# Performance work log

Measured on AMD Instinct MI355X. Metric: run time of the kernel, lower is better.

The kernel has to match this reference:

```python
import jax, jax.numpy as jnp
import numpy as np

B, S, D = 4, 16, 512          # batch, seq, attention_dim
V, T = 32000, 18              # vocab_size, tree_depth
INNER = V - 1                 # internal nodes of Huffman tree


def setup_inputs() -> dict:
    key = jax.random.key(0)
    k_att, k_w, k_idx, k_bit = jax.random.split(key, 4)
    att = jax.random.normal(k_att, (B, S, D), dtype=jnp.float32)
    weight = jax.random.normal(k_w, (INNER, D), dtype=jnp.float32) * 0.02
    path_index = jax.random.randint(k_idx, (V * T,), 0, INNER, dtype=jnp.int64)
    # left/right branch bits: sign=+1,bias=0 -> p ; sign=-1,bias=1 -> 1-p
    bits = jax.random.randint(k_bit, (V * T,), 0, 2).astype(jnp.float32)
    path_sign = 1.0 - 2.0 * bits
    path_bias = bits
    return {
        "att": att,
        "weight": weight,
        "path_index": path_index,
        "path_sign": path_sign,
        "path_bias": path_bias,
        "vocab_size": V,
        "tree_depth": T,
    }


def reference(att, weight, path_index, path_sign, path_bias, vocab_size, tree_depth):
    # h: sigmoid of linear projection onto internal-node vectors  [B,S,INNER]
    h = jax.nn.sigmoid(jnp.einsum("bsd,nd->bsn", att, weight))
    # gather per-(token,depth) internal-node probs, flip via sign/bias
    g = jnp.take(h, path_index, axis=-1) * path_sign + path_bias  # [B,S,V*T]
    Hm = g.reshape(att.shape[0], -1, vocab_size, tree_depth)      # [B,S,V,T]
    return jnp.sum(jnp.log(Hm), axis=-1)                          # [B,S,V]
```

## Files before the change

kernel.cpp:

```cpp
#include <hip/hip_runtime.h>

#define BS    64
#define DDIM  512
#define NV    32000
#define TD    18
#define INNER 31999

typedef __attribute__((ext_vector_type(8))) short short8;
typedef __attribute__((ext_vector_type(4))) float floatx4;

__device__ __forceinline__ float bf16_to_f32(unsigned short u) {
    union { unsigned int i; float f; } v; v.i = ((unsigned int)u) << 16; return v.f;
}
__device__ __forceinline__ unsigned short f32_to_bf16(float f) {
    union { float f; unsigned int i; } v; v.f = f;
    unsigned int r = v.i + 0x7FFFu + ((v.i >> 16) & 1u);
    return (unsigned short)(r >> 16);
}
__device__ __forceinline__ short8 cvt8(float4 a, float4 b) {
    short8 s;
    s[0] = (short)f32_to_bf16(a.x); s[1] = (short)f32_to_bf16(a.y);
    s[2] = (short)f32_to_bf16(a.z); s[3] = (short)f32_to_bf16(a.w);
    s[4] = (short)f32_to_bf16(b.x); s[5] = (short)f32_to_bf16(b.y);
    s[6] = (short)f32_to_bf16(b.z); s[7] = (short)f32_to_bf16(b.w);
    return s;
}

#define IDXB 2250
__global__ __launch_bounds__(256) void prep(
    const int* __restrict__ idx,
    const unsigned int* __restrict__ signbits,
    unsigned short* __restrict__ idx2,
    const float4* __restrict__ att,
    ushort4* __restrict__ attb)
{
    const int b = blockIdx.x;
    if (b < IDXB) {
        const unsigned int* w = (const unsigned int*)idx;
        bool i64 = true;
#pragma unroll
        for (int j = 1; j < 16; j += 2) i64 &= (w[j] == 0u);
        int o = b * 256 + threadIdx.x;
        int val = i64 ? idx[2 * o] : idx[o];
        idx2[o] = (unsigned short)((val << 1) | (int)(signbits[o] >> 31));
    } else {
        int i = (b - IDXB) * 256 + threadIdx.x;
        float4 a = att[i];
        ushort4 r;
        r.x = f32_to_bf16(a.x); r.y = f32_to_bf16(a.y);
        r.z = f32_to_bf16(a.z); r.w = f32_to_bf16(a.w);
        attb[i] = r;
    }
}

__global__ __launch_bounds__(512) void gemm_logsig(
    const ushort4* __restrict__ attb,
    const float* __restrict__ weight,
    unsigned int* __restrict__ pairsT)
{
    __shared__ __align__(16) char As[65536];
    const int tid  = threadIdx.x;
    const int lane = tid & 63;
    const int wave = tid >> 6;
    const int nsub = wave & 3;
    const int msub = wave >> 2;
    const int l15  = lane & 15;
    const int quad = lane >> 4;
    const int B0   = blockIdx.x * 64;

#pragma unroll
    for (int it = 0; it < 8; ++it) {
        int p   = it * 512 + tid;
        int row = p >> 6;
        int c16 = (p & 63) << 4;
        *(uint4*)(As + row * 1024 + (c16 ^ ((row & 7) << 4))) =
            ((const uint4*)attb)[p];
    }
    __syncthreads();

    int brow = B0 + nsub * 16 + l15;
    if (brow > INNER - 1) brow = INNER - 1;
    const float* bbase = weight + (size_t)brow * DDIM + quad * 8;

    const int   r0    = msub * 32 + l15;
    const int   sw    = (r0 & 7) << 4;
    const char* arow0 = As + r0 * 1024;
    const char* arow1 = arow0 + 16 * 1024;
    const int   cbq   = quad * 16;

    floatx4 acc0 = (floatx4){0.f, 0.f, 0.f, 0.f};
    floatx4 acc1 = (floatx4){0.f, 0.f, 0.f, 0.f};
    float4 bA[8], bB[8];

#define LB(BUF, c) { _Pragma("unroll")                                        \
    for (int s = 0; s < 4; ++s) {                                             \
        BUF[2*s]   = *(const float4*)(bbase + (c)*128 + s*32);                \
        BUF[2*s+1] = *(const float4*)(bbase + (c)*128 + s*32 + 4); } }
#define CB(BUF, c) { _Pragma("unroll")                                        \
    for (int s = 0; s < 4; ++s) {                                             \
        short8 bf = cvt8(BUF[2*s], BUF[2*s+1]);                               \
        int cb = ((c)*256 + s*64 + cbq) ^ sw;                                 \
        short8 af0 = *(const short8*)(arow0 + cb);                            \
        short8 af1 = *(const short8*)(arow1 + cb);                            \
        acc0 = __builtin_amdgcn_mfma_f32_16x16x32_bf16(af0, bf, acc0, 0,0,0); \
        acc1 = __builtin_amdgcn_mfma_f32_16x16x32_bf16(af1, bf, acc1, 0,0,0); } }

    LB(bA, 0); LB(bB, 1);
    CB(bA, 0); LB(bA, 2);
    CB(bB, 1); LB(bB, 3);
    CB(bA, 2); CB(bB, 3);
#undef LB
#undef CB

    const int n = B0 + nsub * 16 + l15;
    if (n < INNER) {
        unsigned int* dst = pairsT + ((size_t)n << 6) + msub * 32 + quad * 4;
        floatx4 accs[2] = {acc0, acc1};
#pragma unroll
        for (int mt = 0; mt < 2; ++mt) {
            unsigned int wds[4];
#pragma unroll
            for (int r = 0; r < 4; ++r) {
                float x = accs[mt][r];
                float lp = -(fmaxf(-x, 0.f) + __logf(1.f + __expf(-fabsf(x))));
                float lm = lp - x;
                wds[r] = (unsigned int)f32_to_bf16(lp)
                       | ((unsigned int)f32_to_bf16(lm) << 16);
            }
            uint4 wv; wv.x = wds[0]; wv.y = wds[1]; wv.z = wds[2]; wv.w = wds[3];
            *(uint4*)(dst + mt * 16) = wv;
        }
    }
}

__global__ __launch_bounds__(256) void gather_bs(
    const unsigned int* __restrict__ pairsT,
    const unsigned short* __restrict__ idx2,
    float* __restrict__ out)
{
    __shared__ float tile[32][65];
    const int lane  = threadIdx.x & 63;
    const int wave  = threadIdx.x >> 6;
    const int vbase = blockIdx.x * 32;

#pragma unroll
    for (int i = 0; i < 8; ++i) {
        const int vloc = wave * 8 + i;
        const unsigned short* col = idx2 + (size_t)(vbase + vloc) * TD;
        float s0 = 0.f, s1 = 0.f;
#pragma unroll
        for (int t = 0; t < TD; t += 2) {
            unsigned int e0 = col[t];
            unsigned int e1 = col[t + 1];
            unsigned int p0 = pairsT[((size_t)(e0 >> 1) << 6) + lane];
            unsigned int p1 = pairsT[((size_t)(e1 >> 1) << 6) + lane];
            unsigned short h0 = (e0 & 1u) ? (unsigned short)(p0 >> 16)
                                          : (unsigned short)(p0 & 0xFFFFu);
            unsigned short h1 = (e1 & 1u) ? (unsigned short)(p1 >> 16)
                                          : (unsigned short)(p1 & 0xFFFFu);
            s0 += bf16_to_f32(h0);
            s1 += bf16_to_f32(h1);
        }
        tile[vloc][lane] = s0 + s1;
    }
    __syncthreads();

    const int bs  = threadIdx.x >> 2;
    const int seg = threadIdx.x & 3;
    float4 r0, r1;
    r0.x = tile[seg * 8 + 0][bs]; r0.y = tile[seg * 8 + 1][bs];
    r0.z = tile[seg * 8 + 2][bs]; r0.w = tile[seg * 8 + 3][bs];
    r1.x = tile[seg * 8 + 4][bs]; r1.y = tile[seg * 8 + 5][bs];
    r1.z = tile[seg * 8 + 6][bs]; r1.w = tile[seg * 8 + 7][bs];
    float4* dst = (float4*)(out + (size_t)bs * NV + vbase + seg * 8);
    dst[0] = r0; dst[1] = r1;
}

extern "C" void kernel_launch(void* const* d_in, const int* in_sizes, int n_in,
                              void* d_out, int out_size, void* d_ws, size_t ws_size,
                              hipStream_t stream)
{
    const float*        att    = (const float*)d_in[0];
    const float*        weight = (const float*)d_in[1];
    const int*          pidx   = (const int*)d_in[2];
    const unsigned int* psign  = (const unsigned int*)d_in[3];
    float* out = (float*)d_out;

    char* ws = (char*)d_ws;
    unsigned int*   pairsT = (unsigned int*)ws;
    unsigned short* idx2   = (unsigned short*)(ws + 8192000);
    ushort4*        attb   = (ushort4*)       (ws + 9344000);

    prep<<<IDXB + 32, 256, 0, stream>>>(pidx, psign, idx2, (const float4*)att, attb);
    gemm_logsig<<<500, 512, 0, stream>>>(attb, weight, pairsT);
    gather_bs<<<1000, 256, 0, stream>>>(pairsT, idx2, out);
}
```

Baseline: 137.8 us.

## Fuse prep, GEMM and gather into one cooperative kernel with grid sync

Replaces the three-kernel pipeline (prep, gemm_logsig, gather_bs) with a single cooperative kernel. Each block converts the activations to bf16 straight into LDS, runs the GEMM plus log-sigmoid, waits at a grid-wide sync, then runs the gather. The gather now decodes the int64 path indices and sign bits itself into LDS, and each block handles 64 vocab columns. This removes two kernel launches and the round trips through workspace for the idx2 and attb buffers. In exchange, every block redundantly converts the full activation tensor and pays for a grid barrier. If the cooperative launch fails, the code falls back to two ordinary kernels.

```diff
diff --git a/kernel.cpp b/kernel.cpp
--- a/kernel.cpp
+++ b/kernel.cpp
@@ -1,10 +1,14 @@
 #include <hip/hip_runtime.h>
+#include <hip/hip_cooperative_groups.h>
+
+namespace cg = cooperative_groups;
 
 #define BS    64
 #define DDIM  512
 #define NV    32000
 #define TD    18
 #define INNER 31999
+#define GRID  500
 
 typedef __attribute__((ext_vector_type(8))) short short8;
 typedef __attribute__((ext_vector_type(4))) float floatx4;
@@ -26,57 +30,34 @@
     return s;
 }
 
-#define IDXB 2250
-__global__ __launch_bounds__(256) void prep(
-    const int* __restrict__ idx,
-    const unsigned int* __restrict__ signbits,
-    unsigned short* __restrict__ idx2,
-    const float4* __restrict__ att,
-    ushort4* __restrict__ attb)
-{
-    const int b = blockIdx.x;
-    if (b < IDXB) {
-        const unsigned int* w = (const unsigned int*)idx;
-        bool i64 = true;
-#pragma unroll
-        for (int j = 1; j < 16; j += 2) i64 &= (w[j] == 0u);
-        int o = b * 256 + threadIdx.x;
-        int val = i64 ? idx[2 * o] : idx[o];
-        idx2[o] = (unsigned short)((val << 1) | (int)(signbits[o] >> 31));
-    } else {
-        int i = (b - IDXB) * 256 + threadIdx.x;
-        float4 a = att[i];
+__device__ __forceinline__ void stage_att(const float* __restrict__ att,
+                                          char* As, int tid)
+{
+    const float4* a4 = (const float4*)att;
+#pragma unroll
+    for (int it = 0; it < 16; ++it) {
+        int p   = it * 512 + tid;
+        float4 a = a4[p];
+        int row = p >> 7;
+        int c8  = (p & 127) << 3;
         ushort4 r;
         r.x = f32_to_bf16(a.x); r.y = f32_to_bf16(a.y);
         r.z = f32_to_bf16(a.z); r.w = f32_to_bf16(a.w);
-        attb[i] = r;
-    }
-}
-
-__global__ __launch_bounds__(512) void gemm_logsig(
-    const ushort4* __restrict__ attb,
-    const float* __restrict__ weight,
-    unsigned int* __restrict__ pairsT)
-{
-    __shared__ __align__(16) char As[65536];
-    const int tid  = threadIdx.x;
+        *(ushort4*)(As + row * 1024 + (c8 ^ ((row & 7) << 4))) = r;
+    }
+}
+
+__device__ __forceinline__ void gemm_phase(
+    const char* As, const float* __restrict__ weight,
+    unsigned int* __restrict__ pairsT, int bid, int tid)
+{
     const int lane = tid & 63;
     const int wave = tid >> 6;
     const int nsub = wave & 3;
     const int msub = wave >> 2;
     const int l15  = lane & 15;
     const int quad = lane >> 4;
-    const int B0   = blockIdx.x * 64;
-
-#pragma unroll
-    for (int it = 0; it < 8; ++it) {
-        int p   = it * 512 + tid;
-        int row = p >> 6;
-        int c16 = (p & 63) << 4;
-        *(uint4*)(As + row * 1024 + (c16 ^ ((row & 7) << 4))) =
-            ((const uint4*)attb)[p];
-    }
-    __syncthreads();
+    const int B0   = bid * 64;
 
     int brow = B0 + nsub * 16 + l15;
     if (brow > INNER - 1) brow = INNER - 1;
@@ -133,20 +114,33 @@
     }
 }
 
-__global__ __launch_bounds__(256) void gather_bs(
+__device__ __forceinline__ void gather_phase(
     const unsigned int* __restrict__ pairsT,
-    const unsigned short* __restrict__ idx2,
-    float* __restrict__ out)
-{
-    __shared__ float tile[32][65];
-    const int lane  = threadIdx.x & 63;
-    const int wave  = threadIdx.x >> 6;
-    const int vbase = blockIdx.x * 32;
+    const int* __restrict__ idx, const unsigned int* __restrict__ signbits,
+    float* __restrict__ out, char* lds, int bid, int tid)
+{
+    unsigned int* eLDS = (unsigned int*)lds;
+    float (*tile)[65]  = (float(*)[65])(lds + 4608);
+    const int lane  = tid & 63;
+    const int wave  = tid >> 6;
+    const int vbase = bid * 64;
+
+    const unsigned int* w = (const unsigned int*)idx;
+    bool i64 = true;
+#pragma unroll
+    for (int j = 1; j < 16; j += 2) i64 &= (w[j] == 0u);
+
+    for (int q = tid; q < 1152; q += 512) {
+        int g = vbase * TD + q;
+        int val = i64 ? idx[2 * g] : idx[g];
+        eLDS[q] = ((unsigned int)val << 1) | (signbits[g] >> 31);
+    }
+    __syncthreads();
 
 #pragma unroll
     for (int i = 0; i < 8; ++i) {
         const int vloc = wave * 8 + i;
-        const unsigned short* col = idx2 + (size_t)(vbase + vloc) * TD;
+        const unsigned int* col = eLDS + vloc * TD;
         float s0 = 0.f, s1 = 0.f;
 #pragma unroll
         for (int t = 0; t < TD; t += 2) {
@@ -165,8 +159,8 @@
     }
     __syncthreads();
 
-    const int bs  = threadIdx.x >> 2;
-    const int seg = threadIdx.x & 3;
+    const int bs  = tid >> 3;
+    const int seg = tid & 7;
     float4 r0, r1;
     r0.x = tile[seg * 8 + 0][bs]; r0.y = tile[seg * 8 + 1][bs];
     r0.z = tile[seg * 8 + 2][bs]; r0.w = tile[seg * 8 + 3][bs];
@@ -176,6 +170,43 @@
     dst[0] = r0; dst[1] = r1;
 }
 
+__global__ __launch_bounds__(512, 4) void fused(
+    const float* __restrict__ att, const float* __restrict__ weight,
+    unsigned int* __restrict__ pairsT,
+    const int* __restrict__ idx, const unsigned int* __restrict__ signbits,
+    float* __restrict__ out)
+{
+    __shared__ __align__(16) char lds[65536];
+    const int tid = threadIdx.x;
+    const int bid = blockIdx.x;
+
+    stage_att(att, lds, tid);
+    __syncthreads();
+    gemm_phase(lds, weight, pairsT, bid, tid);
+
+    cg::this_grid().sync();
+
+    gather_phase(pairsT, idx, signbits, out, lds, bid, tid);
+}
+
+__global__ __launch_bounds__(512, 4) void k_gemm(
+    const float* __restrict__ att, const float* __restrict__ weight,
+    unsigned int* __restrict__ pairsT)
+{
+    __shared__ __align__(16) char lds[65536];
+    stage_att(att, lds, threadIdx.x);
+    __syncthreads();
+    gemm_phase(lds, weight, pairsT, blockIdx.x, threadIdx.x);
+}
+__global__ __launch_bounds__(512) void k_gather(
+    const unsigned int* __restrict__ pairsT,
+    const int* __restrict__ idx, const unsigned int* __restrict__ signbits,
+    float* __restrict__ out)
+{
+    __shared__ __align__(16) char lds[21248];
+    gather_phase(pairsT, idx, signbits, out, lds, blockIdx.x, threadIdx.x);
+}
+
 extern "C" void kernel_launch(void* const* d_in, const int* in_sizes, int n_in,
                               void* d_out, int out_size, void* d_ws, size_t ws_size,
                               hipStream_t stream)
@@ -186,12 +217,14 @@
     const unsigned int* psign  = (const unsigned int*)d_in[3];
     float* out = (float*)d_out;
 
-    char* ws = (char*)d_ws;
-    unsigned int*   pairsT = (unsigned int*)ws;
-    unsigned short* idx2   = (unsigned short*)(ws + 8192000);
-    ushort4*        attb   = (ushort4*)       (ws + 9344000);
-
-    prep<<<IDXB + 32, 256, 0, stream>>>(pidx, psign, idx2, (const float4*)att, attb);
-    gemm_logsig<<<500, 512, 0, stream>>>(attb, weight, pairsT);
-    gather_bs<<<1000, 256, 0, stream>>>(pairsT, idx2, out);
-}
+    unsigned int* pairsT = (unsigned int*)d_ws;
+
+    void* kargs[] = { (void*)&att, (void*)&weight, (void*)&pairsT,
+                      (void*)&pidx, (void*)&psign, (void*)&out };
+    hipError_t err = hipLaunchCooperativeKernel(
+        (const void*)fused, dim3(GRID), dim3(512), kargs, 0, stream);
+    if (err != hipSuccess) {
+        k_gemm  <<<GRID, 512, 0, stream>>>(att, weight, pairsT);
+        k_gather<<<GRID, 512, 0, stream>>>(pairsT, pidx, psign, out);
+    }
+}
```

Measured after the change: 215.2 us. 1.56x slower.
